# Optimization experiments

Hardware: AMD Instinct MI355X
Metric: run time of the kernel (lower is better)

Reference implementation:

```python
import jax, jax.numpy as jnp
import numpy as np

N = 50000
E = 800000
D_IN = 64
D_OUT = 64
D_EDGE = 16


def setup_inputs() -> dict:
    key = jax.random.key(0)
    ks = jax.random.split(key, 10)
    x = jax.random.normal(ks[0], (N, D_IN), dtype=jnp.float32)
    edge_index = jax.random.randint(ks[1], (2, E), 0, N, dtype=jnp.int64)
    edge_attr = jax.random.normal(ks[2], (E, D_EDGE), dtype=jnp.float32)
    s = 1.0 / np.sqrt(D_EDGE)
    We = jax.random.uniform(ks[3], (D_EDGE, D_IN), minval=-s, maxval=s, dtype=jnp.float32)
    be = jax.random.uniform(ks[4], (D_IN,), minval=-s, maxval=s, dtype=jnp.float32)
    s1 = 1.0 / np.sqrt(D_IN)
    W1 = jax.random.uniform(ks[5], (D_IN, D_OUT), minval=-s1, maxval=s1, dtype=jnp.float32)
    b1 = jax.random.uniform(ks[6], (D_OUT,), minval=-s1, maxval=s1, dtype=jnp.float32)
    s2 = 1.0 / np.sqrt(D_OUT)
    W2 = jax.random.uniform(ks[7], (D_OUT, D_OUT), minval=-s2, maxval=s2, dtype=jnp.float32)
    b2 = jax.random.uniform(ks[8], (D_OUT,), minval=-s2, maxval=s2, dtype=jnp.float32)
    return {"x": x, "edge_index": edge_index, "edge_attr": edge_attr,
            "We": We, "be": be, "W1": W1, "b1": b1, "W2": W2, "b2": b2}


def reference(x, edge_index, edge_attr, We, be, W1, b1, W2, b2):
    src = edge_index[0]  # message source j
    dst = edge_index[1]  # aggregation target i (PyG source_to_target flow)
    # per-edge message: relu(x_j + lin_edge(edge_attr))
    msg = jax.nn.relu(x[src] + edge_attr @ We + be)  # [E, D_IN]
    # scatter-sum aggregation at target nodes
    agg = jax.ops.segment_sum(msg, dst, num_segments=N)  # [N, D_IN]
    eps = 0.0  # GINEConv default, train_eps=False
    h = (1.0 + eps) * x + agg
    # mlp: Linear -> ReLU -> Linear (dropout p=0.0 -> identity)
    out = jax.nn.relu(h @ W1 + b1) @ W2 + b2
    return out
```

## Files before the change

### kernel.cpp

```cpp
#include <hip/hip_runtime.h>
#include <hip/hip_bf16.h>

#define NN 50000
#define EE 800000

__device__ __forceinline__ float bflo(unsigned u) { return __uint_as_float(u << 16); }
__device__ __forceinline__ float bfhi(unsigned u) { return __uint_as_float(u & 0xffff0000u); }

__global__ void detect_dtype(const unsigned* __restrict__ xw, int* __restrict__ flag) {
    if (threadIdx.x == 0 && blockIdx.x == 0) {
        int cnt = 0;
        for (int i = 0; i < 64; i++) {
            unsigned e = (xw[i] >> 7) & 0xFFu;
            if (e >= 100u && e <= 140u) cnt++;
        }
        *flag = (cnt >= 32) ? 1 : 0;
    }
}

template <bool BF16>
__device__ __forceinline__ void edge_body(
    const void* __restrict__ xv, const int* __restrict__ ei,
    const void* __restrict__ eav, const void* __restrict__ Wev,
    const void* __restrict__ bev, float* __restrict__ agg)
{
    const int tid = threadIdx.x;
    const int d   = tid & 63;
    const int sub = tid >> 6;

    const int oddor = ei[1] | ei[3] | ei[5] | ei[7] | ei[9] | ei[11] | ei[13] | ei[15];
    const bool idx64 = (oddor == 0);
    const long long* __restrict__ ei64 = (const long long*)ei;

    float we[16];
    float bed;
    if constexpr (BF16) {
        const __hip_bfloat16* We = (const __hip_bfloat16*)Wev;
        const __hip_bfloat16* be = (const __hip_bfloat16*)bev;
#pragma unroll
        for (int k = 0; k < 16; k++) we[k] = __bfloat162float(We[k * 64 + d]);
        bed = __bfloat162float(be[d]);
    } else {
        const float* We = (const float*)Wev;
        const float* be = (const float*)bev;
#pragma unroll
        for (int k = 0; k < 16; k++) we[k] = We[k * 64 + d];
        bed = be[d];
    }

    const int stride = gridDim.x * 4;
    for (int e = blockIdx.x * 4 + sub; e < EE; e += stride) {
        int src, dst;
        if (idx64) { src = (int)ei64[e]; dst = (int)ei64[EE + e]; }
        else       { src = ei[e];        dst = ei[EE + e]; }

        float a[16];
        if constexpr (BF16) {
            const uint4* row = (const uint4*)((const __hip_bfloat16*)eav + (size_t)e * 16);
            const uint4 p0 = row[0];
            const uint4 p1 = row[1];
            a[0]=bflo(p0.x); a[1]=bfhi(p0.x); a[2]=bflo(p0.y); a[3]=bfhi(p0.y);
            a[4]=bflo(p0.z); a[5]=bfhi(p0.z); a[6]=bflo(p0.w); a[7]=bfhi(p0.w);
            a[8]=bflo(p1.x); a[9]=bfhi(p1.x); a[10]=bflo(p1.y); a[11]=bfhi(p1.y);
            a[12]=bflo(p1.z); a[13]=bfhi(p1.z); a[14]=bflo(p1.w); a[15]=bfhi(p1.w);
        } else {
            const float4* row = (const float4*)((const float*)eav + (size_t)e * 16);
            const float4 q0 = row[0], q1 = row[1], q2 = row[2], q3 = row[3];
            a[0]=q0.x; a[1]=q0.y; a[2]=q0.z; a[3]=q0.w;
            a[4]=q1.x; a[5]=q1.y; a[6]=q1.z; a[7]=q1.w;
            a[8]=q2.x; a[9]=q2.y; a[10]=q2.z; a[11]=q2.w;
            a[12]=q3.x; a[13]=q3.y; a[14]=q3.z; a[15]=q3.w;
        }

        float acc = bed;
#pragma unroll
        for (int k = 0; k < 16; k++) acc = fmaf(a[k], we[k], acc);

        float xs;
        if constexpr (BF16) xs = __bfloat162float(((const __hip_bfloat16*)xv)[(size_t)src * 64 + d]);
        else                xs = ((const float*)xv)[(size_t)src * 64 + d];

        float msg = fmaxf(acc + xs, 0.0f);
        atomicAdd(&agg[(size_t)dst * 64 + d], msg);
    }
}

__global__ __launch_bounds__(256) void edge_agg_kernel(
    const void* x, const int* ei, const void* ea,
    const void* We, const void* be, float* agg, const int* flag)
{
    if (*flag) edge_body<true>(x, ei, ea, We, be, agg);
    else       edge_body<false>(x, ei, ea, We, be, agg);
}

template <bool BF16>
__device__ __forceinline__ void mlp_body(
    const void* __restrict__ xv, const float* __restrict__ agg,
    const void* __restrict__ W1v, const void* __restrict__ b1v,
    const void* __restrict__ W2v, const void* __restrict__ b2v,
    void* __restrict__ outv)
{
    __shared__ float sh[4][64];
    __shared__ float st[4][64];
    const int tid = threadIdx.x;
    const int d   = tid & 63;
    const int w   = tid >> 6;

    float w1c[64], w2c[64], b1d, b2d;
    if constexpr (BF16) {
        const __hip_bfloat16* W1 = (const __hip_bfloat16*)W1v;
        const __hip_bfloat16* W2 = (const __hip_bfloat16*)W2v;
#pragma unroll
        for (int k = 0; k < 64; k++) {
            w1c[k] = __bfloat162float(W1[k * 64 + d]);
            w2c[k] = __bfloat162float(W2[k * 64 + d]);
        }
        b1d = __bfloat162float(((const __hip_bfloat16*)b1v)[d]);
        b2d = __bfloat162float(((const __hip_bfloat16*)b2v)[d]);
    } else {
        const float* W1 = (const float*)W1v;
        const float* W2 = (const float*)W2v;
#pragma unroll
        for (int k = 0; k < 64; k++) {
            w1c[k] = W1[k * 64 + d];
            w2c[k] = W2[k * 64 + d];
        }
        b1d = ((const float*)b1v)[d];
        b2d = ((const float*)b2v)[d];
    }

    const int stride = gridDim.x * 4;
    const int iters  = (NN + stride - 1) / stride;
    int node = blockIdx.x * 4 + w;
    for (int it = 0; it < iters; it++, node += stride) {
        const bool valid = node < NN;
        if (valid) {
            float xs;
            if constexpr (BF16) xs = __bfloat162float(((const __hip_bfloat16*)xv)[(size_t)node * 64 + d]);
            else                xs = ((const float*)xv)[(size_t)node * 64 + d];
            sh[w][d] = xs + agg[(size_t)node * 64 + d];
        }
        __syncthreads();

        float t = b1d;
        const float4* hv = (const float4*)sh[w];
#pragma unroll
        for (int k = 0; k < 16; k++) {
            const float4 hq = hv[k];
            t = fmaf(hq.x, w1c[4 * k],     t);
            t = fmaf(hq.y, w1c[4 * k + 1], t);
            t = fmaf(hq.z, w1c[4 * k + 2], t);
            t = fmaf(hq.w, w1c[4 * k + 3], t);
        }
        t = fmaxf(t, 0.0f);
        st[w][d] = t;
        __syncthreads();

        float o = b2d;
        const float4* tv = (const float4*)st[w];
#pragma unroll
        for (int k = 0; k < 16; k++) {
            const float4 tq = tv[k];
            o = fmaf(tq.x, w2c[4 * k],     o);
            o = fmaf(tq.y, w2c[4 * k + 1], o);
            o = fmaf(tq.z, w2c[4 * k + 2], o);
            o = fmaf(tq.w, w2c[4 * k + 3], o);
        }
        if (valid) {
            if constexpr (BF16) ((__hip_bfloat16*)outv)[(size_t)node * 64 + d] = __float2bfloat16(o);
            else                ((float*)outv)[(size_t)node * 64 + d] = o;
        }
    }
}

__global__ __launch_bounds__(256) void mlp_kernel(
    const void* x, const float* agg,
    const void* W1, const void* b1, const void* W2, const void* b2,
    void* out, const int* flag)
{
    if (*flag) mlp_body<true>(x, agg, W1, b1, W2, b2, out);
    else       mlp_body<false>(x, agg, W1, b1, W2, b2, out);
}

extern "C" void kernel_launch(void* const* d_in, const int* in_sizes, int n_in,
                              void* d_out, int out_size, void* d_ws, size_t ws_size,
                              hipStream_t stream) {
    const void* x          = d_in[0];
    const int*  edge_index = (const int*)d_in[1];
    const void* edge_attr  = d_in[2];
    const void* We         = d_in[3];
    const void* be         = d_in[4];
    const void* W1         = d_in[5];
    const void* b1         = d_in[6];
    const void* W2         = d_in[7];
    const void* b2         = d_in[8];

    float* agg = (float*)d_ws;
    int*   flag = (int*)((char*)d_ws + (size_t)NN * 64 * sizeof(float));

    hipMemsetAsync(agg, 0, (size_t)NN * 64 * sizeof(float), stream);
    hipLaunchKernelGGL(detect_dtype, dim3(1), dim3(64), 0, stream,
                       (const unsigned*)x, flag);
    hipLaunchKernelGGL(edge_agg_kernel, dim3(4096), dim3(256), 0, stream,
                       x, edge_index, edge_attr, We, be, agg, flag);
    hipLaunchKernelGGL(mlp_kernel, dim3(2048), dim3(256), 0, stream,
                       x, agg, W1, b1, W2, b2, d_out, flag);
}
```

Measured before the change: 325.9 us.

## Replace atomic scatter with CSR counting-sort gather fused into the MLP

```diff
diff --git a/kernel.cpp b/kernel.cpp
--- a/kernel.cpp
+++ b/kernel.cpp
@@ -18,87 +18,75 @@
     }
 }
 
+__device__ __forceinline__ bool ei_is64(const int* __restrict__ ei) {
+    const int oddor = ei[1] | ei[3] | ei[5] | ei[7] | ei[9] | ei[11] | ei[13] | ei[15];
+    return oddor == 0;
+}
+
+__global__ __launch_bounds__(256) void hist_kernel(const int* __restrict__ ei,
+                                                   int* __restrict__ counts) {
+    const bool idx64 = ei_is64(ei);
+    const long long* __restrict__ ei64 = (const long long*)ei;
+    int e = blockIdx.x * 256 + threadIdx.x;
+    if (e < EE) {
+        int dst = idx64 ? (int)ei64[EE + e] : ei[EE + e];
+        atomicAdd(&counts[dst], 1);
+    }
+}
+
+__global__ __launch_bounds__(1024) void scan_kernel(const int* __restrict__ counts,
+                                                    int* __restrict__ offs,
+                                                    int* __restrict__ cursor) {
+    __shared__ int part[1024];
+    const int t = threadIdx.x;
+    const int C = 49;
+    const int base = t * C;
+    int s = 0;
+    for (int i = 0; i < C; i++) {
+        int idx = base + i;
+        if (idx < NN) s += counts[idx];
+    }
+    part[t] = s;
+    __syncthreads();
+    for (int off = 1; off < 1024; off <<= 1) {
+        int add = (t >= off) ? part[t - off] : 0;
+        __syncthreads();
+        if (t >= off) part[t] += add;
+        __syncthreads();
+    }
+    int running = part[t] - s;
+    for (int i = 0; i < C; i++) {
+        int idx = base + i;
+        if (idx < NN) {
+            offs[idx]   = running;
+            cursor[idx] = running;
+            running += counts[idx];
+        }
+    }
+}
+
+__global__ __launch_bounds__(256) void scatter_kernel(const int* __restrict__ ei,
+                                                      int* __restrict__ cursor,
+                                                      int* __restrict__ perm) {
+    const bool idx64 = ei_is64(ei);
+    const long long* __restrict__ ei64 = (const long long*)ei;
+    int e = blockIdx.x * 256 + threadIdx.x;
+    if (e < EE) {
+        int dst = idx64 ? (int)ei64[EE + e] : ei[EE + e];
+        int pos = atomicAdd(&cursor[dst], 1);
+        perm[pos] = e;
+    }
+}
+
 template <bool BF16>
-__device__ __forceinline__ void edge_body(
+__device__ __forceinline__ void gather_mlp_body(
     const void* __restrict__ xv, const int* __restrict__ ei,
-    const void* __restrict__ eav, const void* __restrict__ Wev,
-    const void* __restrict__ bev, float* __restrict__ agg)
-{
-    const int tid = threadIdx.x;
-    const int d   = tid & 63;
-    const int sub = tid >> 6;
-
-    const int oddor = ei[1] | ei[3] | ei[5] | ei[7] | ei[9] | ei[11] | ei[13] | ei[15];
-    const bool idx64 = (oddor == 0);
-    const long long* __restrict__ ei64 = (const long long*)ei;
-
-    float we[16];
-    float bed;
-    if constexpr (BF16) {
-        const __hip_bfloat16* We = (const __hip_bfloat16*)Wev;
-        const __hip_bfloat16* be = (const __hip_bfloat16*)bev;
-#pragma unroll
-        for (int k = 0; k < 16; k++) we[k] = __bfloat162float(We[k * 64 + d]);
-        bed = __bfloat162float(be[d]);
-    } else {
-        const float* We = (const float*)Wev;
-        const float* be = (const float*)bev;
-#pragma unroll
-        for (int k = 0; k < 16; k++) we[k] = We[k * 64 + d];
-        bed = be[d];
-    }
-
-    const int stride = gridDim.x * 4;
-    for (int e = blockIdx.x * 4 + sub; e < EE; e += stride) {
-        int src, dst;
-        if (idx64) { src = (int)ei64[e]; dst = (int)ei64[EE + e]; }
-        else       { src = ei[e];        dst = ei[EE + e]; }
-
-        float a[16];
-        if constexpr (BF16) {
-            const uint4* row = (const uint4*)((const __hip_bfloat16*)eav + (size_t)e * 16);
-            const uint4 p0 = row[0];
-            const uint4 p1 = row[1];
-            a[0]=bflo(p0.x); a[1]=bfhi(p0.x); a[2]=bflo(p0.y); a[3]=bfhi(p0.y);
-            a[4]=bflo(p0.z); a[5]=bfhi(p0.z); a[6]=bflo(p0.w); a[7]=bfhi(p0.w);
-            a[8]=bflo(p1.x); a[9]=bfhi(p1.x); a[10]=bflo(p1.y); a[11]=bfhi(p1.y);
-            a[12]=bflo(p1.z); a[13]=bfhi(p1.z); a[14]=bflo(p1.w); a[15]=bfhi(p1.w);
-        } else {
-            const float4* row = (const float4*)((const float*)eav + (size_t)e * 16);
-            const float4 q0 = row[0], q1 = row[1], q2 = row[2], q3 = row[3];
-            a[0]=q0.x; a[1]=q0.y; a[2]=q0.z; a[3]=q0.w;
-            a[4]=q1.x; a[5]=q1.y; a[6]=q1.z; a[7]=q1.w;
-            a[8]=q2.x; a[9]=q2.y; a[10]=q2.z; a[11]=q2.w;
-            a[12]=q3.x; a[13]=q3.y; a[14]=q3.z; a[15]=q3.w;
-        }
-
-        float acc = bed;
-#pragma unroll
-        for (int k = 0; k < 16; k++) acc = fmaf(a[k], we[k], acc);
-
-        float xs;
-        if constexpr (BF16) xs = __bfloat162float(((const __hip_bfloat16*)xv)[(size_t)src * 64 + d]);
-        else                xs = ((const float*)xv)[(size_t)src * 64 + d];
-
-        float msg = fmaxf(acc + xs, 0.0f);
-        atomicAdd(&agg[(size_t)dst * 64 + d], msg);
-    }
-}
-
-__global__ __launch_bounds__(256) void edge_agg_kernel(
-    const void* x, const int* ei, const void* ea,
-    const void* We, const void* be, float* agg, const int* flag)
-{
-    if (*flag) edge_body<true>(x, ei, ea, We, be, agg);
-    else       edge_body<false>(x, ei, ea, We, be, agg);
-}
-
-template <bool BF16>
-__device__ __forceinline__ void mlp_body(
-    const void* __restrict__ xv, const float* __restrict__ agg,
+    const void* __restrict__ eav,
+    const void* __restrict__ Wev, const void* __restrict__ bev,
     const void* __restrict__ W1v, const void* __restrict__ b1v,
     const void* __restrict__ W2v, const void* __restrict__ b2v,
-    void* __restrict__ outv)
+    const int* __restrict__ offs, const int* __restrict__ cursor,
+    const int* __restrict__ perm, void* __restrict__ outv)
 {
     __shared__ float sh[4][64];
     __shared__ float st[4][64];
@@ -106,41 +94,92 @@
     const int d   = tid & 63;
     const int w   = tid >> 6;
 
-    float w1c[64], w2c[64], b1d, b2d;
+    const bool idx64 = ei_is64(ei);
+    const long long* __restrict__ ei64 = (const long long*)ei;
+
+    float we[16], bed, w1c[64], w2c[64], b1d, b2d;
     if constexpr (BF16) {
+        const __hip_bfloat16* We = (const __hip_bfloat16*)Wev;
         const __hip_bfloat16* W1 = (const __hip_bfloat16*)W1v;
         const __hip_bfloat16* W2 = (const __hip_bfloat16*)W2v;
+#pragma unroll
+        for (int k = 0; k < 16; k++) we[k] = __bfloat162float(We[k * 64 + d]);
 #pragma unroll
         for (int k = 0; k < 64; k++) {
             w1c[k] = __bfloat162float(W1[k * 64 + d]);
             w2c[k] = __bfloat162float(W2[k * 64 + d]);
         }
+        bed = __bfloat162float(((const __hip_bfloat16*)bev)[d]);
         b1d = __bfloat162float(((const __hip_bfloat16*)b1v)[d]);
         b2d = __bfloat162float(((const __hip_bfloat16*)b2v)[d]);
     } else {
+        const float* We = (const float*)Wev;
         const float* W1 = (const float*)W1v;
         const float* W2 = (const float*)W2v;
+#pragma unroll
+        for (int k = 0; k < 16; k++) we[k] = We[k * 64 + d];
 #pragma unroll
         for (int k = 0; k < 64; k++) {
             w1c[k] = W1[k * 64 + d];
             w2c[k] = W2[k * 64 + d];
         }
+        bed = ((const float*)bev)[d];
         b1d = ((const float*)b1v)[d];
         b2d = ((const float*)b2v)[d];
     }
 
-    const int stride = gridDim.x * 4;
-    const int iters  = (NN + stride - 1) / stride;
-    int node = blockIdx.x * 4 + w;
-    for (int it = 0; it < iters; it++, node += stride) {
-        const bool valid = node < NN;
-        if (valid) {
-            float xs;
-            if constexpr (BF16) xs = __bfloat162float(((const __hip_bfloat16*)xv)[(size_t)node * 64 + d]);
-            else                xs = ((const float*)xv)[(size_t)node * 64 + d];
-            sh[w][d] = xs + agg[(size_t)node * 64 + d];
-        }
-        __syncthreads();
+    const int nwaves = gridDim.x * 4;
+    for (int node = blockIdx.x * 4 + w; node < NN; node += nwaves) {
+        const int start = offs[node];
+        const int end   = cursor[node];
+        float acc = 0.0f;
+
+        for (int base = start; base < end; base += 64) {
+            int m = end - base;
+            if (m > 64) m = 64;
+            int e = 0, s = 0;
+            if (d < m) {
+                e = perm[base + d];
+                s = idx64 ? (int)ei64[e] : ei[e];
+            }
+            for (int j = 0; j < m; j++) {
+                const int ej = __shfl(e, j);
+                const int sj = __shfl(s, j);
+
+                float a[16];
+                if constexpr (BF16) {
+                    const uint4* row = (const uint4*)((const __hip_bfloat16*)eav + (size_t)ej * 16);
+                    const uint4 p0 = row[0];
+                    const uint4 p1 = row[1];
+                    a[0]=bflo(p0.x); a[1]=bfhi(p0.x); a[2]=bflo(p0.y); a[3]=bfhi(p0.y);
+                    a[4]=bflo(p0.z); a[5]=bfhi(p0.z); a[6]=bflo(p0.w); a[7]=bfhi(p0.w);
+                    a[8]=bflo(p1.x); a[9]=bfhi(p1.x); a[10]=bflo(p1.y); a[11]=bfhi(p1.y);
+                    a[12]=bflo(p1.z); a[13]=bfhi(p1.z); a[14]=bflo(p1.w); a[15]=bfhi(p1.w);
+                } else {
+                    const float4* row = (const float4*)((const float*)eav + (size_t)ej * 16);
+                    const float4 q0 = row[0], q1 = row[1], q2 = row[2], q3 = row[3];
+                    a[0]=q0.x; a[1]=q0.y; a[2]=q0.z; a[3]=q0.w;
+                    a[4]=q1.x; a[5]=q1.y; a[6]=q1.z; a[7]=q1.w;
+                    a[8]=q2.x; a[9]=q2.y; a[10]=q2.z; a[11]=q2.w;
+                    a[12]=q3.x; a[13]=q3.y; a[14]=q3.z; a[15]=q3.w;
+                }
+
+                float macc = bed;
+#pragma unroll
+                for (int k = 0; k < 16; k++) macc = fmaf(a[k], we[k], macc);
+
+                float xs;
+                if constexpr (BF16) xs = __bfloat162float(((const __hip_bfloat16*)xv)[(size_t)sj * 64 + d]);
+                else                xs = ((const float*)xv)[(size_t)sj * 64 + d];
+
+                acc += fmaxf(macc + xs, 0.0f);
+            }
+        }
+
+        float xn;
+        if constexpr (BF16) xn = __bfloat162float(((const __hip_bfloat16*)xv)[(size_t)node * 64 + d]);
+        else                xn = ((const float*)xv)[(size_t)node * 64 + d];
+        sh[w][d] = xn + acc;
 
         float t = b1d;
         const float4* hv = (const float4*)sh[w];
@@ -154,7 +193,6 @@
         }
         t = fmaxf(t, 0.0f);
         st[w][d] = t;
-        __syncthreads();
 
         float o = b2d;
         const float4* tv = (const float4*)st[w];
@@ -166,20 +204,20 @@
             o = fmaf(tq.z, w2c[4 * k + 2], o);
             o = fmaf(tq.w, w2c[4 * k + 3], o);
         }
-        if (valid) {
-            if constexpr (BF16) ((__hip_bfloat16*)outv)[(size_t)node * 64 + d] = __float2bfloat16(o);
-            else                ((float*)outv)[(size_t)node * 64 + d] = o;
-        }
-    }
-}
-
-__global__ __launch_bounds__(256) void mlp_kernel(
-    const void* x, const float* agg,
+        if constexpr (BF16) ((__hip_bfloat16*)outv)[(size_t)node * 64 + d] = __float2bfloat16(o);
+        else                ((float*)outv)[(size_t)node * 64 + d] = o;
+    }
+}
+
+__global__ __launch_bounds__(256) void gather_mlp_kernel(
+    const void* x, const int* ei, const void* ea,
+    const void* We, const void* be,
     const void* W1, const void* b1, const void* W2, const void* b2,
+    const int* offs, const int* cursor, const int* perm,
     void* out, const int* flag)
 {
-    if (*flag) mlp_body<true>(x, agg, W1, b1, W2, b2, out);
-    else       mlp_body<false>(x, agg, W1, b1, W2, b2, out);
+    if (*flag) gather_mlp_body<true >(x, ei, ea, We, be, W1, b1, W2, b2, offs, cursor, perm, out);
+    else       gather_mlp_body<false>(x, ei, ea, We, be, W1, b1, W2, b2, offs, cursor, perm, out);
 }
 
 extern "C" void kernel_launch(void* const* d_in, const int* in_sizes, int n_in,
@@ -195,14 +233,22 @@
     const void* W2         = d_in[7];
     const void* b2         = d_in[8];
 
-    float* agg = (float*)d_ws;
-    int*   flag = (int*)((char*)d_ws + (size_t)NN * 64 * sizeof(float));
-
-    hipMemsetAsync(agg, 0, (size_t)NN * 64 * sizeof(float), stream);
+    int* counts = (int*)d_ws;
+    int* offs   = counts + 50016;
+    int* cursor = offs   + 50016;
+    int* perm   = cursor + 50016;
+    int* flag   = perm   + EE;
+
+    hipMemsetAsync(counts, 0, (size_t)NN * sizeof(int), stream);
     hipLaunchKernelGGL(detect_dtype, dim3(1), dim3(64), 0, stream,
                        (const unsigned*)x, flag);
-    hipLaunchKernelGGL(edge_agg_kernel, dim3(4096), dim3(256), 0, stream,
-                       x, edge_index, edge_attr, We, be, agg, flag);
-    hipLaunchKernelGGL(mlp_kernel, dim3(2048), dim3(256), 0, stream,
-                       x, agg, W1, b1, W2, b2, d_out, flag);
-}
+    hipLaunchKernelGGL(hist_kernel, dim3((EE + 255) / 256), dim3(256), 0, stream,
+                       edge_index, counts);
+    hipLaunchKernelGGL(scan_kernel, dim3(1), dim3(1024), 0, stream,
+                       counts, offs, cursor);
+    hipLaunchKernelGGL(scatter_kernel, dim3((EE + 255) / 256), dim3(256), 0, stream,
+                       edge_index, cursor, perm);
+    hipLaunchKernelGGL(gather_mlp_kernel, dim3(1600), dim3(256), 0, stream,
+                       x, edge_index, edge_attr, We, be, W1, b1, W2, b2,
+                       offs, cursor, perm, d_out, flag);
+}
```

Result: slower. 584.7 us (+79.4%).
